# Optimization experiments

Measured on AMD Instinct MI355X. Metric: run time of the kernel, lower is better.

The kernel has to match this reference:

```python
import jax, jax.numpy as jnp
import numpy as np

B, C, H, W = 2, 256, 64, 64
KEEP = 0.1


def setup_inputs() -> dict:
    key = jax.random.key(0)
    ks = jax.random.split(key, 7)
    s = 0.05  # small init for 1x1-conv weights
    return {
        "x": jax.random.normal(ks[0], (B, C, H, W), dtype=jnp.float32),
        "Wq": jax.random.normal(ks[1], (C, C), dtype=jnp.float32) * s,
        "bq": jax.random.normal(ks[2], (C,), dtype=jnp.float32) * s,
        "Wk": jax.random.normal(ks[3], (C, C), dtype=jnp.float32) * s,
        "bk": jax.random.normal(ks[4], (C,), dtype=jnp.float32) * s,
        "Wv": jax.random.normal(ks[5], (C, C), dtype=jnp.float32) * s,
        "bv": jax.random.normal(ks[6], (C,), dtype=jnp.float32) * s,
    }


def reference(x, Wq, bq, Wk, bk, Wv, bv):
    b, c, h, w = x.shape
    n = h * w

    def proj(Wm, bm):
        # 1x1 conv == per-pixel linear; output as [B, N, C] tokens
        return jnp.einsum('bchw,oc->bhwo', x, Wm).reshape(b, n, c) + bm

    q = proj(Wq, bq)
    k = proj(Wk, bk)
    v = proj(Wv, bv)

    scores = jnp.einsum('bnc,bmc->bnm', q, k) / (c ** 0.5)  # [B, N, N]
    k_keep = max(1, int(KEEP * n))

    vals, idx = jax.lax.top_k(scores, k_keep)  # [B, N, k_keep]
    # softmax over -inf-masked scores == softmax over topk vals scattered into zeros
    probs = jax.nn.softmax(vals, axis=-1)
    attn = jnp.zeros_like(scores).at[
        jnp.arange(b)[:, None, None], jnp.arange(n)[None, :, None], idx
    ].set(probs)

    out = jnp.einsum('bnm,bmc->bnc', attn, v)  # [B, N, C]
    return out.transpose(0, 2, 1).reshape(b, c, h, w)
```

## Files before the change

kernel.cpp:

```cpp
#include <hip/hip_runtime.h>
#include <hip/hip_bf16.h>
#include <math.h>

#define BATCH 2
#define CC    256
#define NN    4096
#define KK    409
#define KCAT  768
#define SCALE 0.0625f
#define PSTRIDE 8192

typedef _Float16 half8 __attribute__((ext_vector_type(8)));
typedef float    floatx4 __attribute__((ext_vector_type(4)));

typedef __attribute__((address_space(3))) unsigned       lds_u32;
typedef __attribute__((address_space(1))) const unsigned glb_u32;
__device__ __forceinline__ void gload16(const void* g, void* l) {
    __builtin_amdgcn_global_load_lds((glb_u32*)g, (lds_u32*)l, 16, 0, 0);
}

__device__ __forceinline__ unsigned fkey(float f) {
    unsigned u = __float_as_uint(f);
    return (u & 0x80000000u) ? ~u : (u | 0x80000000u);
}
__device__ __forceinline__ float keyToF(unsigned k) {
    unsigned u = (k & 0x80000000u) ? (k ^ 0x80000000u) : ~k;
    return __uint_as_float(u);
}

__global__ __launch_bounds__(256) void xpose_wcat_kernel(
        const float* __restrict__ x,
        const float* __restrict__ Wq, const float* __restrict__ Wk,
        const float* __restrict__ Wv,
        _Float16* __restrict__ xcat, _Float16* __restrict__ Wcat) {
    const int t  = threadIdx.x;
    if (blockIdx.y == 4) {
        int idx = (blockIdx.z * 64 + blockIdx.x) * 256 + t;
#pragma unroll
        for (int k = 0; k < 6; k++) {
            int e = idx + k * 32768;
            int mat = e >> 16;
            int o   = (e >> 8) & 255;
            int c   = e & 255;
            const float* W = (mat == 0) ? Wq : (mat == 1) ? Wk : Wv;
            float v = W[o * 256 + c];
            _Float16 hi = (_Float16)v;
            _Float16 lo = (_Float16)(v - (float)hi);
            _Float16* wr = Wcat + ((size_t)(mat * 256 + o)) * KCAT;
            wr[c] = hi; wr[256 + c] = hi; wr[512 + c] = lo;
        }
        return;
    }

    __shared__ float xs[64][68];
    const int n0 = blockIdx.x * 64;
    const int c0 = blockIdx.y * 64;
    const int b  = blockIdx.z;

    {
        const int ci = t >> 2;
        const int j  = (t & 3) * 16;
        const float* xp = x + ((size_t)((b << 8) + c0 + ci)) * NN + n0 + j;
        float4 a0 = ((const float4*)xp)[0];
        float4 a1 = ((const float4*)xp)[1];
        float4 a2 = ((const float4*)xp)[2];
        float4 a3 = ((const float4*)xp)[3];
        *(float4*)&xs[ci][j]      = a0;
        *(float4*)&xs[ci][j + 4]  = a1;
        *(float4*)&xs[ci][j + 8]  = a2;
        *(float4*)&xs[ci][j + 12] = a3;
    }
    __syncthreads();

    const int n = t >> 2;
    const int g0 = t & 3;
    _Float16* xr = xcat + ((size_t)(b * NN + n0 + n)) * KCAT + c0;
#pragma unroll
    for (int gg = 0; gg < 2; gg++) {
        int g = g0 + gg * 4;
        half8 hi, lo;
#pragma unroll
        for (int k = 0; k < 8; k++) {
            float v = xs[g * 8 + k][n];
            _Float16 h = (_Float16)v;
            hi[k] = h;
            lo[k] = (_Float16)(v - (float)h);
        }
        *(half8*)(xr + g * 8)       = hi;
        *(half8*)(xr + 256 + g * 8) = lo;
        *(half8*)(xr + 512 + g * 8) = hi;
    }
}

__global__ __launch_bounds__(256) void proj_gemm(
        const _Float16* __restrict__ xcat, const _Float16* __restrict__ Wcat,
        const float* __restrict__ bq, const float* __restrict__ bk,
        const float* __restrict__ bv,
        _Float16* __restrict__ Qcat, _Float16* __restrict__ Kcat,
        _Float16* __restrict__ Vt) {
    __shared__ _Float16 As[128][64];
    __shared__ _Float16 Bs[128][64];

    const int t    = threadIdx.x;
    const int wave = t >> 6;
    const int l    = t & 63;
    const int wr   = wave >> 1;
    const int wc   = wave & 1;
    const int mat  = blockIdx.z;

    int bym, bxn;
    if (mat < 2) { bym = blockIdx.x >> 1; bxn = blockIdx.x & 1; }
    else         { bym = blockIdx.x & 1;  bxn = blockIdx.x >> 1; }

    const int lr = l >> 3;
    const int gg = (l & 7) ^ lr;

    const _Float16* At;
    const _Float16* Bt;
    if (mat < 2) {
        At = xcat + ((size_t)(bym * 128)) * KCAT;
        Bt = Wcat + ((size_t)(mat * 256 + bxn * 128)) * KCAT;
    } else {
        At = Wcat + ((size_t)(512 + bym * 128)) * KCAT;
        Bt = xcat + ((size_t)(bxn * 128)) * KCAT;
    }
    const size_t lane_off = (size_t)lr * KCAT + gg * 8;

    floatx4 acc[4][4];
#pragma unroll
    for (int i = 0; i < 4; i++)
#pragma unroll
        for (int j = 0; j < 4; j++) acc[i][j] = (floatx4)0.0f;

    const int rowA = l & 15;
    const int sg0  = (l >> 4) ^ (l & 7);
    const int sg1  = sg0 ^ 4;

    for (int kc = 0; kc < KCAT; kc += 64) {
#pragma unroll
        for (int s = 0; s < 4; s++) {
            const int seg = wave * 4 + s;
            gload16(At + (size_t)seg * 8 * KCAT + lane_off + kc, &As[seg * 8][0]);
            gload16(Bt + (size_t)seg * 8 * KCAT + lane_off + kc, &Bs[seg * 8][0]);
        }
        __syncthreads();
#pragma unroll
        for (int ks = 0; ks < 2; ks++) {
            const int sg = ks ? sg1 : sg0;
            half8 af[4], bf[4];
#pragma unroll
            for (int mi = 0; mi < 4; mi++)
                af[mi] = *(const half8*)&As[wr * 64 + mi * 16 + rowA][sg * 8];
#pragma unroll
            for (int ni = 0; ni < 4; ni++)
                bf[ni] = *(const half8*)&Bs[wc * 64 + ni * 16 + rowA][sg * 8];
#pragma unroll
            for (int mi = 0; mi < 4; mi++)
#pragma unroll
                for (int ni = 0; ni < 4; ni++)
                    acc[mi][ni] = __builtin_amdgcn_mfma_f32_16x16x32_f16(
                        af[mi], bf[ni], acc[mi][ni], 0, 0, 0);
        }
        __syncthreads();
    }

    if (mat < 2) {
        const float* bias = (mat == 0) ? bq : bk;
        _Float16* Out = (mat == 0) ? Qcat : Kcat;
#pragma unroll
        for (int ni = 0; ni < 4; ni++) {
            int ch = bxn * 128 + wc * 64 + ni * 16 + (l & 15);
            float bb = bias[ch];
#pragma unroll
            for (int mi = 0; mi < 4; mi++)
#pragma unroll
                for (int rg = 0; rg < 4; rg++) {
                    int token = bym * 128 + wr * 64 + mi * 16 + (l >> 4) * 4 + rg;
                    float v = acc[mi][ni][rg] + bb;
                    _Float16 hi = (_Float16)v;
                    _Float16 lo = (_Float16)(v - (float)hi);
                    _Float16* p = Out + (size_t)token * KCAT + ch;
                    if (mat == 0) { p[0] = hi; p[256] = lo; p[512] = hi; }
                    else          { p[0] = hi; p[256] = hi; p[512] = lo; }
                }
        }
    } else {
#pragma unroll
        for (int mi = 0; mi < 4; mi++)
#pragma unroll
            for (int rg = 0; rg < 4; rg++) {
                int ch = bym * 128 + wr * 64 + mi * 16 + (l >> 4) * 4 + rg;
                float bb = bv[ch];
#pragma unroll
                for (int ni = 0; ni < 4; ni++) {
                    int col = bxn * 128 + wc * 64 + ni * 16 + (l & 15);
                    int b = col >> 12, n = col & 4095;
                    Vt[((size_t)((b << 8) + ch)) * NN + n] =
                        (_Float16)(acc[mi][ni][rg] + bb);
                }
            }
    }
}

__global__ __launch_bounds__(512, 2) void score_gemm(
        const _Float16* __restrict__ Qcat, const _Float16* __restrict__ Kcat,
        float* __restrict__ S) {
    __shared__ _Float16 As[256][64];
    __shared__ _Float16 Bs[256][64];

    const int t    = threadIdx.x;
    const int wave = t >> 6;
    const int l    = t & 63;
    const int wr   = wave >> 1;
    const int wc   = wave & 1;

    const int id  = blockIdx.x;
    const int sc  = id & 7;
    const int j   = id >> 3;
    const int b   = sc & 1;
    const int scq = sc >> 1;
    const int bxn = ((scq & 1) << 3) + (j & 7);
    const int bym = ((scq >> 1) << 3) + (j >> 3);

    const int lr = l >> 3;
    const int gg = (l & 7) ^ lr;

    const _Float16* At = Qcat + ((size_t)((b << 12) + bym * 256)) * KCAT;
    const _Float16* Bt = Kcat + ((size_t)((b << 12) + bxn * 256)) * KCAT;
    const size_t lane_off = (size_t)lr * KCAT + gg * 8;

    floatx4 acc[4][8];
#pragma unroll
    for (int i = 0; i < 4; i++)
#pragma unroll
        for (int jj = 0; jj < 8; jj++) acc[i][jj] = (floatx4)0.0f;

    const int rowA = l & 15;
    const int sg0  = (l >> 4) ^ (l & 7);
    const int sg1  = sg0 ^ 4;

    for (int kc = 0; kc < KCAT; kc += 64) {
#pragma unroll
        for (int s = 0; s < 4; s++) {
            const int seg = wave * 4 + s;
            gload16(At + (size_t)seg * 8 * KCAT + lane_off + kc, &As[seg * 8][0]);
            gload16(Bt + (size_t)seg * 8 * KCAT + lane_off + kc, &Bs[seg * 8][0]);
        }
        __syncthreads();
#pragma unroll
        for (int ks = 0; ks < 2; ks++) {
            const int sg = ks ? sg1 : sg0;
            half8 af[4], bf[8];
#pragma unroll
            for (int mi = 0; mi < 4; mi++)
                af[mi] = *(const half8*)&As[wr * 64 + mi * 16 + rowA][sg * 8];
#pragma unroll
            for (int ni = 0; ni < 8; ni++)
                bf[ni] = *(const half8*)&Bs[wc * 128 + ni * 16 + rowA][sg * 8];
#pragma unroll
            for (int mi = 0; mi < 4; mi++)
#pragma unroll
                for (int ni = 0; ni < 8; ni++)
                    acc[mi][ni] = __builtin_amdgcn_mfma_f32_16x16x32_f16(
                        af[mi], bf[ni], acc[mi][ni], 0, 0, 0);
        }
        __syncthreads();
    }

    float* Sb = S + ((size_t)b << 24);
#pragma unroll
    for (int mi = 0; mi < 4; mi++)
#pragma unroll
        for (int ni = 0; ni < 8; ni++) {
            int col = bxn * 256 + wc * 128 + ni * 16 + (l & 15);
#pragma unroll
            for (int rg = 0; rg < 4; rg++) {
                int row = bym * 256 + wr * 64 + mi * 16 + (l >> 4) * 4 + rg;
                Sb[((size_t)row << 12) + col] = acc[mi][ni][rg] * SCALE;
            }
        }
}

__global__ __launch_bounds__(256) void select_scatter(
        const float* __restrict__ S, _Float16* __restrict__ P) {
    __shared__ unsigned hist[256];
    __shared__ unsigned scan[256];
    __shared__ unsigned candKey[NN];
    __shared__ unsigned wred[4];
    __shared__ float    fmn[4], fmx[4], wsum[4];
    __shared__ unsigned sh_d, sh_cntgt, sh_T;
    __shared__ int      sh_ncand, sh_need;

    const int t = threadIdx.x;
    const int l = t & 63;
    const int w = t >> 6;

    float    val[16];
    unsigned ukey[16];
    {
        const float*  Srow = S + ((size_t)blockIdx.x << 12);
        const float4* sp   = (const float4*)(Srow + t * 16);
#pragma unroll
        for (int jj = 0; jj < 4; jj++) {
            float4 v = sp[jj];
            val[jj * 4 + 0] = v.x; val[jj * 4 + 1] = v.y;
            val[jj * 4 + 2] = v.z; val[jj * 4 + 3] = v.w;
        }
#pragma unroll
        for (int j = 0; j < 16; j++) ukey[j] = fkey(val[j]);
    }

    float lmin = val[0], lmax = val[0];
#pragma unroll
    for (int j = 1; j < 16; j++) {
        lmin = fminf(lmin, val[j]); lmax = fmaxf(lmax, val[j]);
    }
#pragma unroll
    for (int off = 32; off > 0; off >>= 1) {
        float a = __shfl_down(lmin, off);
        float b = __shfl_down(lmax, off);
        if (l + off < 64) { lmin = fminf(lmin, a); lmax = fmaxf(lmax, b); }
    }
    if (l == 0) { fmn[w] = lmin; fmx[w] = lmax; }

    hist[t] = 0u;
    if (t == 0) sh_ncand = 0;
    __syncthreads();
    const float fmin = fminf(fminf(fmn[0], fmn[1]), fminf(fmn[2], fmn[3]));
    const float fmax = fmaxf(fmaxf(fmx[0], fmx[1]), fmaxf(fmx[2], fmx[3]));
    const float range = fmax - fmin;
    const float bscale = (range > 1e-20f) ? 255.0f / range : 0.0f;

    auto binOf = [&](float v) -> int {
        int bin = (int)((v - fmin) * bscale);
        return bin < 0 ? 0 : (bin > 255 ? 255 : bin);
    };

#pragma unroll
    for (int j = 0; j < 16; j++) atomicAdd(&hist[binOf(val[j])], 1u);
    __syncthreads();

    int rem = KK;

    auto find_digit = [&](int remv) {
        unsigned v = hist[t];
#pragma unroll
        for (int off = 1; off < 64; off <<= 1) {
            unsigned o = __shfl_down(v, off);
            if (l + off < 64) v += o;
        }
        if (l == 0) wred[w] = v;
        __syncthreads();
        unsigned add = 0u;
#pragma unroll
        for (int w2 = 0; w2 < 4; w2++) if (w2 > w) add += wred[w2];
        scan[t] = v + add;
        __syncthreads();
        unsigned sufd  = scan[t];
        unsigned sufd1 = (t < 255) ? scan[t + 1] : 0u;
        if (sufd >= (unsigned)remv && sufd1 < (unsigned)remv) {
            sh_d = (unsigned)t; sh_cntgt = sufd1;
        }
        __syncthreads();
    };

    find_digit(rem);
    const int dbin = (int)sh_d;
    rem -= (int)sh_cntgt;

#pragma unroll
    for (int j = 0; j < 16; j++) {
        if (binOf(val[j]) == dbin) {
            int slot = atomicAdd(&sh_ncand, 1);
            candKey[slot] = ukey[j];
        }
    }
    __syncthreads();
    const int nc = sh_ncand;

    if (nc <= 64) {
        if (w == 0) {
            unsigned kl = (l < nc) ? candKey[l] : 0u;
            int r = 0, g = 0;
            for (int j = 0; j < 64; j++) {
                unsigned kj = __shfl(kl, j);
                bool gt = kj > kl;
                g += gt ? 1 : 0;
                r += (gt || (kj == kl && j < l)) ? 1 : 0;
            }
            if (r == rem - 1) { sh_T = kl; sh_need = rem - g; }
        }
    } else {
        unsigned prefix = 0u;
        int rem2 = rem;
        for (int pass = 0; pass < 4; pass++) {
            const int shift = 24 - 8 * pass;
            hist[t] = 0u;
            __syncthreads();
            for (int i = t; i < nc; i += 256) {
                unsigned u2 = candKey[i];
                if (pass == 0 || (u2 >> (shift + 8)) == (prefix >> (shift + 8)))
                    atomicAdd(&hist[(u2 >> shift) & 255u], 1u);
            }
            __syncthreads();
            find_digit(rem2);
            prefix |= (sh_d << shift);
            rem2 -= (int)sh_cntgt;
        }
        if (t == 0) { sh_T = prefix; sh_need = rem2; }
    }
    __syncthreads();
    const unsigned T = sh_T;
    const int need = sh_need;
    const float mT = keyToF(T);

    int eqc = 0;
#pragma unroll
    for (int j = 0; j < 16; j++) if (ukey[j] == T) eqc++;
    int vinc = eqc;
#pragma unroll
    for (int off = 1; off < 64; off <<= 1) {
        int o = __shfl_up(vinc, off);
        if (l >= off) vinc += o;
    }
    if (l == 63) wred[w] = (unsigned)vinc;
    __syncthreads();
    int addlow = 0;
#pragma unroll
    for (int w2 = 0; w2 < 4; w2++) if (w2 < w) addlow += (int)wred[w2];
    const int eqexcl = vinc - eqc + addlow;

    float pv[16];
    float le = 0.f;
#pragma unroll
    for (int j = 0; j < 16; j++) {
        float e = 0.f;
        if (ukey[j] > T) { e = __expf(val[j] - mT); le += e; }
        pv[j] = e;
    }
    if (eqc) {
        int seen = 0;
#pragma unroll
        for (int j = 0; j < 16; j++) {
            if (ukey[j] == T) {
                if (eqexcl + seen < need) { pv[j] = 1.0f; le += 1.0f; }
                seen++;
            }
        }
    }

#pragma unroll
    for (int off = 32; off > 0; off >>= 1) {
        float o = __shfl_down(le, off);
        if (l + off < 64) le += o;
    }
    if (l == 0) wsum[w] = le;
    __syncthreads();
    const float inv = 1.0f / (wsum[0] + wsum[1] + wsum[2] + wsum[3]);

    half8 ra, rb;
#pragma unroll
    for (int j = 0; j < 8; j++) {
        ra[j] = (_Float16)(pv[j] * inv);
        rb[j] = (_Float16)(pv[j + 8] * inv);
    }
    _Float16* Pr = P + (size_t)blockIdx.x * PSTRIDE + t * 16;
    *(half8*)Pr       = ra;
    *(half8*)(Pr + 8) = rb;
}

__global__ __launch_bounds__(256) void av_gemm(
        const _Float16* __restrict__ Vt, const _Float16* __restrict__ P,
        float* __restrict__ out) {
    __shared__ _Float16 As0[64][64], As1[64][64];
    __shared__ _Float16 Bs0[64][64], Bs1[64][64];

    const int t    = threadIdx.x;
    const int wave = t >> 6;
    const int l    = t & 63;
    const int wr   = wave >> 1;
    const int wc   = wave & 1;
    const int bxn  = blockIdx.x;
    const int byc  = blockIdx.y;
    const int b    = blockIdx.z;

    const int lr = l >> 3;
    const int gg = (l & 7) ^ lr;

    const _Float16* At = Vt + ((size_t)((b << 8) + byc * 64)) * NN;
    const _Float16* Bt = P + ((size_t)(b * NN + bxn * 64)) * PSTRIDE;
    const size_t lane_offA = (size_t)lr * NN + gg * 8;
    const size_t lane_offB = (size_t)lr * PSTRIDE + gg * 8;

    floatx4 acc[2][2];
#pragma unroll
    for (int i = 0; i < 2; i++)
#pragma unroll
        for (int j = 0; j < 2; j++) acc[i][j] = (floatx4)0.0f;

    const int rowA   = l & 15;
    const int sgbase = (l >> 4) ^ (l & 7);

    for (int kc = 0; kc < NN; kc += 128) {
#pragma unroll
        for (int s = 0; s < 2; s++) {
            const int seg = wave * 2 + s;
            gload16(At + (size_t)seg * 8 * NN + lane_offA + kc,           &As0[seg * 8][0]);
            gload16(At + (size_t)seg * 8 * NN + lane_offA + kc + 64,      &As1[seg * 8][0]);
            gload16(Bt + (size_t)seg * 8 * PSTRIDE + lane_offB + kc,      &Bs0[seg * 8][0]);
            gload16(Bt + (size_t)seg * 8 * PSTRIDE + lane_offB + kc + 64, &Bs1[seg * 8][0]);
        }
        __syncthreads();
#pragma unroll
        for (int st = 0; st < 4; st++) {
            const _Float16 (*Ap)[64] = (st < 2) ? As0 : As1;
            const _Float16 (*Bp)[64] = (st < 2) ? Bs0 : Bs1;
            const int sg = sgbase ^ ((st & 1) ? 4 : 0);
            half8 af[2], bf[2];
#pragma unroll
            for (int mi = 0; mi < 2; mi++)
                af[mi] = *(const half8*)&Ap[wr * 32 + mi * 16 + rowA][sg * 8];
#pragma unroll
            for (int ni = 0; ni < 2; ni++)
                bf[ni] = *(const half8*)&Bp[wc * 32 + ni * 16 + rowA][sg * 8];
#pragma unroll
            for (int mi = 0; mi < 2; mi++)
#pragma unroll
                for (int ni = 0; ni < 2; ni++)
                    acc[mi][ni] = __builtin_amdgcn_mfma_f32_16x16x32_f16(
                        af[mi], bf[ni], acc[mi][ni], 0, 0, 0);
        }
        __syncthreads();
    }

#pragma unroll
    for (int mi = 0; mi < 2; mi++)
#pragma unroll
        for (int ni = 0; ni < 2; ni++) {
            int col = bxn * 64 + wc * 32 + ni * 16 + (l & 15);
#pragma unroll
            for (int rg = 0; rg < 4; rg++) {
                int row = byc * 64 + wr * 32 + mi * 16 + (l >> 4) * 4 + rg;
                out[((size_t)((b << 8) + row) << 12) + col] = acc[mi][ni][rg];
            }
        }
}

extern "C" void kernel_launch(void* const* d_in, const int* in_sizes, int n_in,
                              void* d_out, int out_size, void* d_ws, size_t ws_size,
                              hipStream_t stream) {
    const float* x  = (const float*)d_in[0];
    const float* Wq = (const float*)d_in[1];
    const float* bq = (const float*)d_in[2];
    const float* Wk = (const float*)d_in[3];
    const float* bk = (const float*)d_in[4];
    const float* Wv = (const float*)d_in[5];
    const float* bv = (const float*)d_in[6];
    float* out = (float*)d_out;

    char* ws = (char*)d_ws;
    _Float16* Wcat = (_Float16*)ws;
    _Float16* Qcat = (_Float16*)(ws + 1179648);
    _Float16* Kcat = (_Float16*)(ws + 1179648 + 12582912);
    _Float16* Vt   = (_Float16*)(ws + 1179648 + 2 * 12582912);
    float*    S    = (float*)   (ws + 1179648 + 2 * 12582912 + 4194304);
    _Float16* xcat = (_Float16*)S;
    _Float16* P    = (_Float16*)S;

    xpose_wcat_kernel<<<dim3(64, 5, BATCH), 256, 0, stream>>>(x, Wq, Wk, Wv,
                                                              xcat, Wcat);
    proj_gemm<<<dim3(128, 1, 3), 256, 0, stream>>>(xcat, Wcat, bq, bk, bv,
                                                   Qcat, Kcat, Vt);
    score_gemm<<<dim3(512, 1, 1), 512, 0, stream>>>(Qcat, Kcat, S);
    select_scatter<<<BATCH * NN, 256, 0, stream>>>(S, P);
    av_gemm<<<dim3(64, 4, BATCH), 256, 0, stream>>>(Vt, P, out);
}
```

Baseline: 243.4 us.

## Double-buffer LDS tiles in score GEMM and interleave MFMA with barriers

The score GEMM now keeps two LDS buffers for the Q and K tiles, so the global-to-LDS loads for the next k-step are issued before computing on the current one. The MFMA loop is split into four quarters with explicit barriers, waitcnts and s_setprio so waves stagger their LDS reads and matrix work. The goal is to hide global load latency that was previously exposed between two __syncthreads. Doubling LDS to 128KB per block likely cuts occupancy from the requested two blocks per CU to one, and the extra barriers add synchronisation cost.

```diff
diff --git a/kernel.cpp b/kernel.cpp
--- a/kernel.cpp
+++ b/kernel.cpp
@@ -205,8 +205,8 @@
 __global__ __launch_bounds__(512, 2) void score_gemm(
         const _Float16* __restrict__ Qcat, const _Float16* __restrict__ Kcat,
         float* __restrict__ S) {
-    __shared__ _Float16 As[256][64];
-    __shared__ _Float16 Bs[256][64];
+    __shared__ _Float16 As[2][256][64];
+    __shared__ _Float16 Bs[2][256][64];
 
     const int t    = threadIdx.x;
     const int wave = t >> 6;
@@ -237,34 +237,70 @@
 
     const int rowA = l & 15;
     const int sg0  = (l >> 4) ^ (l & 7);
-    const int sg1  = sg0 ^ 4;
-
-    for (int kc = 0; kc < KCAT; kc += 64) {
-#pragma unroll
-        for (int s = 0; s < 4; s++) {
-            const int seg = wave * 4 + s;
-            gload16(At + (size_t)seg * 8 * KCAT + lane_off + kc, &As[seg * 8][0]);
-            gload16(Bt + (size_t)seg * 8 * KCAT + lane_off + kc, &Bs[seg * 8][0]);
-        }
-        __syncthreads();
+
+#pragma unroll
+    for (int s = 0; s < 4; s++) {
+        const int seg = wave * 4 + s;
+        gload16(At + (size_t)seg * 8 * KCAT + lane_off, &As[0][seg * 8][0]);
+        gload16(Bt + (size_t)seg * 8 * KCAT + lane_off, &Bs[0][seg * 8][0]);
+    }
+    asm volatile("s_waitcnt vmcnt(0)" ::: "memory");
+    __builtin_amdgcn_s_barrier();
+
+    for (int kt = 0; kt < 12; ++kt) {
+        const int cur = kt & 1;
+
+        if (kt < 11) {
+            const int kc = (kt + 1) * 64;
+#pragma unroll
+            for (int s = 0; s < 4; s++) {
+                const int seg = wave * 4 + s;
+                gload16(At + (size_t)seg * 8 * KCAT + lane_off + kc,
+                        &As[cur ^ 1][seg * 8][0]);
+                gload16(Bt + (size_t)seg * 8 * KCAT + lane_off + kc,
+                        &Bs[cur ^ 1][seg * 8][0]);
+            }
+        }
+
+        half8 af[4][2];
 #pragma unroll
         for (int ks = 0; ks < 2; ks++) {
-            const int sg = ks ? sg1 : sg0;
-            half8 af[4], bf[8];
+            const int sg = sg0 ^ (ks << 2);
 #pragma unroll
             for (int mi = 0; mi < 4; mi++)
-                af[mi] = *(const half8*)&As[wr * 64 + mi * 16 + rowA][sg * 8];
-#pragma unroll
-            for (int ni = 0; ni < 8; ni++)
-                bf[ni] = *(const half8*)&Bs[wc * 128 + ni * 16 + rowA][sg * 8];
-#pragma unroll
-            for (int mi = 0; mi < 4; mi++)
-#pragma unroll
-                for (int ni = 0; ni < 8; ni++)
-                    acc[mi][ni] = __builtin_amdgcn_mfma_f32_16x16x32_f16(
-                        af[mi], bf[ni], acc[mi][ni], 0, 0, 0);
-        }
-        __syncthreads();
+                af[mi][ks] =
+                    *(const half8*)&As[cur][wr * 64 + mi * 16 + rowA][sg * 8];
+        }
+
+#pragma unroll
+        for (int q = 0; q < 4; q++) {
+            half8 bf[2][2];
+#pragma unroll
+            for (int ks = 0; ks < 2; ks++) {
+                const int sg = sg0 ^ (ks << 2);
+#pragma unroll
+                for (int nj = 0; nj < 2; nj++)
+                    bf[nj][ks] = *(const half8*)
+                        &Bs[cur][wc * 128 + (q * 2 + nj) * 16 + rowA][sg * 8];
+            }
+            __builtin_amdgcn_s_barrier();
+            asm volatile("s_waitcnt lgkmcnt(0)" ::: "memory");
+            __builtin_amdgcn_sched_barrier(0);
+            __builtin_amdgcn_s_setprio(1);
+#pragma unroll
+            for (int ks = 0; ks < 2; ks++)
+#pragma unroll
+                for (int mi = 0; mi < 4; mi++)
+#pragma unroll
+                    for (int nj = 0; nj < 2; nj++)
+                        acc[mi][q * 2 + nj] = __builtin_amdgcn_mfma_f32_16x16x32_f16(
+                            af[mi][ks], bf[nj][ks], acc[mi][q * 2 + nj], 0, 0, 0);
+            __builtin_amdgcn_s_setprio(0);
+            if (q < 3) __builtin_amdgcn_s_barrier();
+        }
+
+        asm volatile("s_waitcnt vmcnt(0)" ::: "memory");
+        __builtin_amdgcn_s_barrier();
     }
 
     float* Sb = S + ((size_t)b << 24);
```

Measured after the change: 246.6 us. Within noise of the previous version (+1.3%).

## Double-buffer LDS tiles in projection and AV GEMMs to overlap loads with MFMA

Applied to the files above, without the earlier changes.

Both the projection GEMM and the attention-value GEMM now stage the next K-tile into a second LDS buffer while MFMAs consume the current one, using a prologue load and a ping-pong index. Previously each iteration loaded a tile, synchronised, then computed, so global latency was exposed every step. The AV GEMM moves from 128-wide K steps with two halves to 64-wide double-buffered steps. This doubles LDS use in proj_gemm, and the end-of-iteration sync is not shown, so correctness depends on where the remaining barrier sits.

```diff
diff --git a/kernel.cpp b/kernel.cpp
--- a/kernel.cpp
+++ b/kernel.cpp
@@ -98,8 +98,8 @@
         const float* __restrict__ bv,
         _Float16* __restrict__ Qcat, _Float16* __restrict__ Kcat,
         _Float16* __restrict__ Vt) {
-    __shared__ _Float16 As[128][64];
-    __shared__ _Float16 Bs[128][64];
+    __shared__ _Float16 As[2][128][64];
+    __shared__ _Float16 Bs[2][128][64];
 
     const int t    = threadIdx.x;
     const int wave = t >> 6;
@@ -136,24 +136,37 @@
     const int sg0  = (l >> 4) ^ (l & 7);
     const int sg1  = sg0 ^ 4;
 
-    for (int kc = 0; kc < KCAT; kc += 64) {
-#pragma unroll
-        for (int s = 0; s < 4; s++) {
-            const int seg = wave * 4 + s;
-            gload16(At + (size_t)seg * 8 * KCAT + lane_off + kc, &As[seg * 8][0]);
-            gload16(Bt + (size_t)seg * 8 * KCAT + lane_off + kc, &Bs[seg * 8][0]);
-        }
-        __syncthreads();
+#pragma unroll
+    for (int s = 0; s < 4; s++) {
+        const int seg = wave * 4 + s;
+        gload16(At + (size_t)seg * 8 * KCAT + lane_off, &As[0][seg * 8][0]);
+        gload16(Bt + (size_t)seg * 8 * KCAT + lane_off, &Bs[0][seg * 8][0]);
+    }
+    __syncthreads();
+
+    for (int kt = 0; kt < 12; ++kt) {
+        const int cur = kt & 1;
+        if (kt < 11) {
+            const int kc = (kt + 1) * 64;
+#pragma unroll
+            for (int s = 0; s < 4; s++) {
+                const int seg = wave * 4 + s;
+                gload16(At + (size_t)seg * 8 * KCAT + lane_off + kc,
+                        &As[cur ^ 1][seg * 8][0]);
+                gload16(Bt + (size_t)seg * 8 * KCAT + lane_off + kc,
+                        &Bs[cur ^ 1][seg * 8][0]);
+            }
+        }
 #pragma unroll
         for (int ks = 0; ks < 2; ks++) {
             const int sg = ks ? sg1 : sg0;
             half8 af[4], bf[4];
 #pragma unroll
             for (int mi = 0; mi < 4; mi++)
-                af[mi] = *(const half8*)&As[wr * 64 + mi * 16 + rowA][sg * 8];
+                af[mi] = *(const half8*)&As[cur][wr * 64 + mi * 16 + rowA][sg * 8];
 #pragma unroll
             for (int ni = 0; ni < 4; ni++)
-                bf[ni] = *(const half8*)&Bs[wc * 64 + ni * 16 + rowA][sg * 8];
+                bf[ni] = *(const half8*)&Bs[cur][wc * 64 + ni * 16 + rowA][sg * 8];
 #pragma unroll
             for (int mi = 0; mi < 4; mi++)
 #pragma unroll
@@ -472,8 +485,8 @@
 __global__ __launch_bounds__(256) void av_gemm(
         const _Float16* __restrict__ Vt, const _Float16* __restrict__ P,
         float* __restrict__ out) {
-    __shared__ _Float16 As0[64][64], As1[64][64];
-    __shared__ _Float16 Bs0[64][64], Bs1[64][64];
+    __shared__ _Float16 As[2][64][64];
+    __shared__ _Float16 Bs[2][64][64];
 
     const int t    = threadIdx.x;
     const int wave = t >> 6;
@@ -501,28 +514,37 @@
     const int rowA   = l & 15;
     const int sgbase = (l >> 4) ^ (l & 7);
 
-    for (int kc = 0; kc < NN; kc += 128) {
-#pragma unroll
-        for (int s = 0; s < 2; s++) {
-            const int seg = wave * 2 + s;
-            gload16(At + (size_t)seg * 8 * NN + lane_offA + kc,           &As0[seg * 8][0]);
-            gload16(At + (size_t)seg * 8 * NN + lane_offA + kc + 64,      &As1[seg * 8][0]);
-            gload16(Bt + (size_t)seg * 8 * PSTRIDE + lane_offB + kc,      &Bs0[seg * 8][0]);
-            gload16(Bt + (size_t)seg * 8 * PSTRIDE + lane_offB + kc + 64, &Bs1[seg * 8][0]);
-        }
-        __syncthreads();
-#pragma unroll
-        for (int st = 0; st < 4; st++) {
-            const _Float16 (*Ap)[64] = (st < 2) ? As0 : As1;
-            const _Float16 (*Bp)[64] = (st < 2) ? Bs0 : Bs1;
-            const int sg = sgbase ^ ((st & 1) ? 4 : 0);
+#pragma unroll
+    for (int s = 0; s < 2; s++) {
+        const int seg = wave * 2 + s;
+        gload16(At + (size_t)seg * 8 * NN + lane_offA,      &As[0][seg * 8][0]);
+        gload16(Bt + (size_t)seg * 8 * PSTRIDE + lane_offB, &Bs[0][seg * 8][0]);
+    }
+    __syncthreads();
+
+    for (int kt = 0; kt < 64; ++kt) {
+        const int cur = kt & 1;
+        if (kt < 63) {
+            const int kc = (kt + 1) * 64;
+#pragma unroll
+            for (int s = 0; s < 2; s++) {
+                const int seg = wave * 2 + s;
+                gload16(At + (size_t)seg * 8 * NN + lane_offA + kc,
+                        &As[cur ^ 1][seg * 8][0]);
+                gload16(Bt + (size_t)seg * 8 * PSTRIDE + lane_offB + kc,
+                        &Bs[cur ^ 1][seg * 8][0]);
+            }
+        }
+#pragma unroll
+        for (int st = 0; st < 2; st++) {
+            const int sg = sgbase ^ (st ? 4 : 0);
             half8 af[2], bf[2];
 #pragma unroll
             for (int mi = 0; mi < 2; mi++)
-                af[mi] = *(const half8*)&Ap[wr * 32 + mi * 16 + rowA][sg * 8];
+                af[mi] = *(const half8*)&As[cur][wr * 32 + mi * 16 + rowA][sg * 8];
 #pragma unroll
             for (int ni = 0; ni < 2; ni++)
-                bf[ni] = *(const half8*)&Bp[wc * 32 + ni * 16 + rowA][sg * 8];
+                bf[ni] = *(const half8*)&Bs[cur][wc * 32 + ni * 16 + rowA][sg * 8];
 #pragma unroll
             for (int mi = 0; mi < 2; mi++)
 #pragma unroll
```

After: 251.8 us. 1.03x slower.
